# Kernel optimization log

Measured on AMD Instinct MI355X. Metric: run time of the kernel, lower is better.

## Reference

```python
import jax, jax.numpy as jnp
import numpy as np

D_MODEL = 1024
NUM_HEADS = 16
D_HEAD = D_MODEL // NUM_HEADS
SCALE = float(np.sqrt(D_HEAD))
NEG = -1e9


def setup_inputs() -> dict:
    key = jax.random.key(0)
    ks = jax.random.split(key, 4)
    B, K = 4, 1024
    tokens = jax.random.normal(ks[0], (B, K, D_MODEL), dtype=jnp.float32)
    token_mask = jnp.ones((B, K), dtype=jnp.int32)
    W_qkv = jax.random.normal(ks[1], (D_MODEL, 3 * D_MODEL), dtype=jnp.float32) * 0.02
    b_qkv = jnp.zeros((3 * D_MODEL,), dtype=jnp.float32)
    W_proj = jax.random.normal(ks[2], (D_MODEL, D_MODEL), dtype=jnp.float32) * 0.02
    b_proj = jnp.zeros((D_MODEL,), dtype=jnp.float32)
    return {"tokens": tokens, "token_mask": token_mask, "W_qkv": W_qkv,
            "b_qkv": b_qkv, "W_proj": W_proj, "b_proj": b_proj}


def reference(tokens, token_mask, W_qkv, b_qkv, W_proj, b_proj):
    B, K, D = tokens.shape
    H, dh = NUM_HEADS, D // NUM_HEADS
    # QKV projection: (B, K, 3D) -> (3, B, H, K, dh)
    qkv = (tokens @ W_qkv + b_qkv).reshape(B, K, 3, H, dh)
    qkv = jnp.transpose(qkv, (2, 0, 3, 1, 4))
    q, k, v = qkv[0], qkv[1], qkv[2]
    # scaled scores (B, H, K, K)
    attn = jnp.einsum('bhqd,bhkd->bhqk', q, k) / SCALE
    # additive padding mask: valid iff both query and key positions valid
    tm = token_mask.astype(attn.dtype)
    m = tm[:, None, None, :] * tm[:, None, :, None]          # (B,1,K,K)
    attn = attn + (1.0 - jnp.clip(m, 0.0)) * NEG
    attn = jax.nn.softmax(attn, axis=-1)
    # weighted values, merge heads
    out = jnp.einsum('bhqk,bhkd->bhqd', attn, v)
    out = jnp.transpose(out, (0, 2, 1, 3)).reshape(B, K, D)
    out = out @ W_proj + b_proj
    tokens_out = tokens + out                                 # residual (dropout=0)
    attn_out = attn.mean(axis=1)                              # (B, K, K)
    return tokens_out, attn_out
```

## Files before the change

### kernel.cpp

```cpp
#include <hip/hip_runtime.h>
#include <hip/hip_bf16.h>
#include <math.h>

#define SEQ   1024
#define DM    1024
#define NH    16
#define DH    64
#define INV_SCALE 0.125f
#define NEGBIG   -1e9f
#define MASKPEN 80.0f

typedef __attribute__((ext_vector_type(8))) __bf16 bf16x8;
typedef __attribute__((ext_vector_type(4))) float floatx4;
typedef unsigned short ushort_t;

__device__ __forceinline__ floatx4 mfma16(bf16x8 a, bf16x8 b, floatx4 c) {
    return __builtin_amdgcn_mfma_f32_16x16x32_bf16(a, b, c, 0, 0, 0);
}

__device__ __forceinline__ ushort_t f2bf(float f) {
    unsigned int u = __float_as_uint(f);
    u += 0x7fffu + ((u >> 16) & 1u);
    return (ushort_t)(u >> 16);
}

__device__ __forceinline__ void gload_lds16(const void* g, void* l) {
    __builtin_amdgcn_global_load_lds(
        (const __attribute__((address_space(1))) unsigned int*)g,
        (__attribute__((address_space(3))) unsigned int*)l, 16, 0, 0);
}

__global__ __launch_bounds__(256) void k_cast(const float* __restrict__ src,
                                              ushort_t* __restrict__ dst) {
    int i = (blockIdx.x * 256 + threadIdx.x) * 8;
    float4 a = *(const float4*)(src + i);
    float4 b = *(const float4*)(src + i + 4);
    union { ushort_t s[8]; uint4 v; } pk;
    pk.s[0] = f2bf(a.x); pk.s[1] = f2bf(a.y); pk.s[2] = f2bf(a.z); pk.s[3] = f2bf(a.w);
    pk.s[4] = f2bf(b.x); pk.s[5] = f2bf(b.y); pk.s[6] = f2bf(b.z); pk.s[7] = f2bf(b.w);
    *(uint4*)(dst + i) = pk.v;
}

__global__ __launch_bounds__(256) void k_transpose(const float* __restrict__ src,
                                                   ushort_t* __restrict__ dst,
                                                   int R, int C) {
    __shared__ ushort_t tile[32][33];
    int bx = blockIdx.x * 32;
    int by = blockIdx.y * 32;
    for (int i = threadIdx.y; i < 32; i += 8)
        tile[i][threadIdx.x] = f2bf(src[(size_t)(by + i) * C + bx + threadIdx.x]);
    __syncthreads();
    for (int i = threadIdx.y; i < 32; i += 8)
        dst[(size_t)(bx + i) * R + by + threadIdx.x] = tile[threadIdx.x][i];
}

__device__ __forceinline__ void gemm128_body(const ushort_t* __restrict__ A,
                                             const ushort_t* __restrict__ Bt,
                                             int m0, int n0, int Kd,
                                             floatx4 acc[4][4], ushort_t* smem) {
    int tid  = threadIdx.x;
    int wave = tid >> 6, lane = tid & 63;
    int l15 = lane & 15, quad = lane >> 4;
    int wr = (wave >> 1) * 64, wc = (wave & 1) * 64;
    int rsub = lane >> 2;
    int ksub = (((lane & 3) ^ ((lane >> 3) & 3)) * 8);
    int rsw  = (l15 >> 1) & 3;

    for (int k0 = 0; k0 < Kd; k0 += 32) {
        __syncthreads();
        #pragma unroll
        for (int c = 0; c < 2; ++c) {
            int rbase = wave * 32 + c * 16;
            gload_lds16(A  + (size_t)(m0 + rbase + rsub) * Kd + k0 + ksub,
                        smem + rbase * 32);
            gload_lds16(Bt + (size_t)(n0 + rbase + rsub) * Kd + k0 + ksub,
                        smem + 4096 + rbase * 32);
        }
        __syncthreads();

        bf16x8 af[4], bfr[4];
        #pragma unroll
        for (int i = 0; i < 4; ++i)
            af[i] = *(const bf16x8*)(smem + (wr + i * 16 + l15) * 32 + (quad ^ rsw) * 8);
        #pragma unroll
        for (int j = 0; j < 4; ++j)
            bfr[j] = *(const bf16x8*)(smem + 4096 + (wc + j * 16 + l15) * 32 + (quad ^ rsw) * 8);
        #pragma unroll
        for (int i = 0; i < 4; ++i)
            #pragma unroll
            for (int j = 0; j < 4; ++j)
                acc[i][j] = mfma16(af[i], bfr[j], acc[i][j]);
    }
}

__global__ __launch_bounds__(256, 2) void k_qkv_gemm(const ushort_t* __restrict__ X,
                                                     const ushort_t* __restrict__ Wt,
                                                     const float* __restrict__ bias,
                                                     ushort_t* __restrict__ qb,
                                                     ushort_t* __restrict__ kb,
                                                     ushort_t* __restrict__ vtb) {
    __shared__ ushort_t smem[8192];
    int m0 = blockIdx.y * 128, n0 = blockIdx.x * 128;
    floatx4 acc[4][4];
    #pragma unroll
    for (int i = 0; i < 4; ++i)
        #pragma unroll
        for (int j = 0; j < 4; ++j) acc[i][j] = (floatx4)0.0f;

    gemm128_body(X, Wt, m0, n0, DM, acc, smem);

    int tid = threadIdx.x, wave = tid >> 6, lane = tid & 63;
    int l15 = lane & 15, quad = lane >> 4;
    int wr = (wave >> 1) * 64, wc = (wave & 1) * 64;
    #pragma unroll
    for (int i = 0; i < 4; ++i) {
        int mrow0 = m0 + wr + i * 16 + quad * 4;
        int b = mrow0 >> 10, t0 = mrow0 & 1023;
        #pragma unroll
        for (int j = 0; j < 4; ++j) {
            int n = n0 + wc + j * 16 + l15;
            float bv = bias[n];
            int sec = n >> 10, nn = n & 1023;
            int h = nn >> 6, d = nn & 63;
            if (sec == 2) {
                union { ushort_t s[4]; uint2 v; } pk;
                #pragma unroll
                for (int r = 0; r < 4; ++r) pk.s[r] = f2bf(acc[i][j][r] + bv);
                *(uint2*)(vtb + (((size_t)(b * NH + h) * DH + d) * SEQ + t0)) = pk.v;
            } else {
                ushort_t* dst = (sec == 0) ? qb : kb;
                #pragma unroll
                for (int r = 0; r < 4; ++r)
                    dst[((size_t)(b * NH + h) * SEQ + t0 + r) * DH + d] =
                        f2bf(acc[i][j][r] + bv);
            }
        }
    }
}

__global__ __launch_bounds__(256, 4) void k_attn_flash(const ushort_t* __restrict__ qb,
                                                       const ushort_t* __restrict__ kb,
                                                       const ushort_t* __restrict__ vtb,
                                                       const int* __restrict__ mask,
                                                       float* __restrict__ lbuf,
                                                       ushort_t* __restrict__ ob) {
    __shared__ ushort_t ks[2 * 64 * 64];
    __shared__ ushort_t vs[2 * 64 * 64];
    __shared__ ushort_t ps[4 * 16 * 64];
    int bh = blockIdx.x, qt = blockIdx.y;
    int b = bh >> 4, h = bh & 15;
    int tid = threadIdx.x, wave = tid >> 6, lane = tid & 63;
    int l15 = lane & 15, quad = lane >> 4;
    int qrow = qt * 64 + wave * 16;
    ushort_t* pw = ps + wave * 1024;
    int sw7 = l15 & 7;

    int srow = wave * 16 + (lane >> 3);
    int slog = (lane & 7) ^ (srow & 7);

    const ushort_t* qbase = qb + ((size_t)bh * SEQ + qrow + l15) * DH;
    bf16x8 aq0 = *(const bf16x8*)(qbase + quad * 8);
    bf16x8 aq1 = *(const bf16x8*)(qbase + 32 + quad * 8);

    bf16x8 vones;
    #pragma unroll
    for (int i = 0; i < 8; ++i) vones[i] = (__bf16)1.0f;

    float qp[4];
    #pragma unroll
    for (int r = 0; r < 4; ++r)
        qp[r] = MASKPEN * (float)mask[b * SEQ + qrow + quad * 4 + r];

    floatx4 oacc[4], lacc = (floatx4)0.0f;
    #pragma unroll
    for (int t = 0; t < 4; ++t) oacc[t] = (floatx4)0.0f;

    #pragma unroll
    for (int c = 0; c < 2; ++c) {
        gload_lds16(kb  + ((size_t)bh * SEQ + srow + c * 8) * DH + slog * 8,
                    ks + (wave * 16 + c * 8) * 64);
        gload_lds16(vtb + ((size_t)bh * DH + srow + c * 8) * SEQ + slog * 8,
                    vs + (wave * 16 + c * 8) * 64);
    }

    for (int it = 0; it < SEQ / 64; ++it) {
        int kc = it * 64;
        int sel = it & 1;
        __syncthreads();
        if (it + 1 < SEQ / 64) {
            int nsel = sel ^ 1;
            #pragma unroll
            for (int c = 0; c < 2; ++c) {
                gload_lds16(kb  + ((size_t)bh * SEQ + kc + 64 + srow + c * 8) * DH + slog * 8,
                            ks + nsel * 4096 + (wave * 16 + c * 8) * 64);
                gload_lds16(vtb + ((size_t)bh * DH + srow + c * 8) * SEQ + kc + 64 + slog * 8,
                            vs + nsel * 4096 + (wave * 16 + c * 8) * 64);
            }
        }
        const ushort_t* kcur = ks + sel * 4096;
        const ushort_t* vcur = vs + sel * 4096;

        floatx4 s[4];
        #pragma unroll
        for (int j = 0; j < 4; ++j) {
            int row = j * 16 + l15;
            bf16x8 k0 = *(const bf16x8*)(kcur + row * 64 + ((quad ^ sw7) * 8));
            bf16x8 k1 = *(const bf16x8*)(kcur + row * 64 + (((quad + 4) ^ sw7) * 8));
            s[j] = mfma16(aq0, k0, (floatx4)0.0f);
            s[j] = mfma16(aq1, k1, s[j]);
        }
        #pragma unroll
        for (int j = 0; j < 4; ++j) {
            float km = (float)mask[b * SEQ + kc + j * 16 + l15];
            #pragma unroll
            for (int r = 0; r < 4; ++r) {
                float arg = s[j][r] * INV_SCALE + (qp[r] * km - MASKPEN);
                float p = __expf(arg);
                int rd = quad * 4 + r;
                int ch = (2 * j + (l15 >> 3)) ^ (rd & 7);
                pw[rd * 64 + ch * 8 + (l15 & 7)] = f2bf(p);
            }
        }
        bf16x8 pa0 = *(const bf16x8*)(pw + l15 * 64 + ((quad ^ sw7) * 8));
        bf16x8 pa1 = *(const bf16x8*)(pw + l15 * 64 + (((quad + 4) ^ sw7) * 8));
        lacc = mfma16(pa0, vones, lacc);
        lacc = mfma16(pa1, vones, lacc);
        #pragma unroll
        for (int t = 0; t < 4; ++t) {
            bf16x8 bv0 = *(const bf16x8*)(vcur + (t * 16 + l15) * 64 + ((quad ^ sw7) * 8));
            bf16x8 bv1 = *(const bf16x8*)(vcur + (t * 16 + l15) * 64 + (((quad + 4) ^ sw7) * 8));
            oacc[t] = mfma16(pa0, bv0, oacc[t]);
            oacc[t] = mfma16(pa1, bv1, oacc[t]);
        }
    }
    float invl[4];
    #pragma unroll
    for (int r = 0; r < 4; ++r) invl[r] = 1.0f / lacc[r];
    #pragma unroll
    for (int t = 0; t < 4; ++t)
        #pragma unroll
        for (int r = 0; r < 4; ++r)
            ob[((size_t)b * SEQ + qrow + quad * 4 + r) * DM + h * DH + t * 16 + l15] =
                f2bf(oacc[t][r] * invl[r]);
    if (l15 == 0) {
        #pragma unroll
        for (int r = 0; r < 4; ++r)
            lbuf[(size_t)bh * SEQ + qrow + quad * 4 + r] = invl[r];
    }
}

__global__ __launch_bounds__(256, 4) void k_attn_avg(const ushort_t* __restrict__ qb,
                                                     const ushort_t* __restrict__ kb,
                                                     const int* __restrict__ mask,
                                                     const float* __restrict__ lbuf,
                                                     float* __restrict__ attn_out) {
    __shared__ ushort_t ks[2 * 64 * 64];
    int bx = blockIdx.x;
    int b  = bx >> 8;
    int qt = (bx >> 4) & 15;
    int kt = bx & 15;
    int tid = threadIdx.x, wave = tid >> 6, lane = tid & 63;
    int l15 = lane & 15, quad = lane >> 4;
    int q0 = qt * 64 + wave * 16;
    int kbase = kt * 64;
    int sw7 = l15 & 7;

    int srow = wave * 16 + (lane >> 3);
    int slog = (lane & 7) ^ (srow & 7);
    int bh0 = b * NH;

    float qp[4], km[4];
    #pragma unroll
    for (int r = 0; r < 4; ++r)
        qp[r] = MASKPEN * (float)mask[b * SEQ + q0 + quad * 4 + r];
    #pragma unroll
    for (int j = 0; j < 4; ++j)
        km[j] = (float)mask[b * SEQ + kbase + j * 16 + l15];

    floatx4 aacc[4];
    #pragma unroll
    for (int j = 0; j < 4; ++j) aacc[j] = (floatx4)0.0f;

    #pragma unroll
    for (int c = 0; c < 2; ++c)
        gload_lds16(kb + ((size_t)bh0 * SEQ + kbase + srow + c * 8) * DH + slog * 8,
                    ks + (wave * 16 + c * 8) * 64);
    const ushort_t* qp0 = qb + ((size_t)bh0 * SEQ + q0 + l15) * DH;
    bf16x8 aq0 = *(const bf16x8*)(qp0 + quad * 8);
    bf16x8 aq1 = *(const bf16x8*)(qp0 + 32 + quad * 8);
    floatx4 il = *(const floatx4*)(lbuf + (size_t)bh0 * SEQ + q0 + quad * 4);
    __syncthreads();

    for (int h = 0; h < NH; ++h) {
        ushort_t* cur = ks + (h & 1) * 4096;
        ushort_t* nxt = ks + ((h + 1) & 1) * 4096;
        if (h + 1 < NH) {
            #pragma unroll
            for (int c = 0; c < 2; ++c)
                gload_lds16(kb + ((size_t)(bh0 + h + 1) * SEQ + kbase + srow + c * 8) * DH + slog * 8,
                            nxt + (wave * 16 + c * 8) * 64);
        }
        bf16x8 caq0 = aq0, caq1 = aq1;
        floatx4 cil = il;
        if (h + 1 < NH) {
            const ushort_t* qpn = qb + ((size_t)(bh0 + h + 1) * SEQ + q0 + l15) * DH;
            aq0 = *(const bf16x8*)(qpn + quad * 8);
            aq1 = *(const bf16x8*)(qpn + 32 + quad * 8);
            il = *(const floatx4*)(lbuf + (size_t)(bh0 + h + 1) * SEQ + q0 + quad * 4);
        }
        cil *= 0.0625f;

        #pragma unroll
        for (int j = 0; j < 4; ++j) {
            int row = j * 16 + l15;
            bf16x8 k0 = *(const bf16x8*)(cur + row * 64 + ((quad ^ sw7) * 8));
            bf16x8 k1 = *(const bf16x8*)(cur + row * 64 + (((quad + 4) ^ sw7) * 8));
            floatx4 s = mfma16(caq0, k0, (floatx4)0.0f);
            s = mfma16(caq1, k1, s);
            #pragma unroll
            for (int r = 0; r < 4; ++r) {
                float arg = s[r] * INV_SCALE + (qp[r] * km[j] - MASKPEN);
                aacc[j][r] += __expf(arg) * cil[r];
            }
        }
        __syncthreads();
    }
    #pragma unroll
    for (int j = 0; j < 4; ++j)
        #pragma unroll
        for (int r = 0; r < 4; ++r)
            attn_out[((size_t)b * SEQ + q0 + quad * 4 + r) * SEQ +
                     kbase + j * 16 + l15] = aacc[j][r];
}

__global__ __launch_bounds__(256, 2) void k_proj(const ushort_t* __restrict__ ob,
                                                 const ushort_t* __restrict__ Wpt,
                                                 const float* __restrict__ bias,
                                                 const float* __restrict__ tokens,
                                                 float* __restrict__ out) {
    __shared__ ushort_t smem[8192];
    int m0 = blockIdx.y * 128, n0 = blockIdx.x * 128;
    floatx4 acc[4][4];
    #pragma unroll
    for (int i = 0; i < 4; ++i)
        #pragma unroll
        for (int j = 0; j < 4; ++j) acc[i][j] = (floatx4)0.0f;

    gemm128_body(ob, Wpt, m0, n0, DM, acc, smem);

    int tid = threadIdx.x, wave = tid >> 6, lane = tid & 63;
    int l15 = lane & 15, quad = lane >> 4;
    int wr = (wave >> 1) * 64, wc = (wave & 1) * 64;
    #pragma unroll
    for (int i = 0; i < 4; ++i) {
        int m0r = m0 + wr + i * 16 + quad * 4;
        #pragma unroll
        for (int j = 0; j < 4; ++j) {
            int n = n0 + wc + j * 16 + l15;
            float bv = bias[n];
            #pragma unroll
            for (int r = 0; r < 4; ++r) {
                size_t idx = (size_t)(m0r + r) * DM + n;
                out[idx] = acc[i][j][r] + bv + tokens[idx];
            }
        }
    }
}

extern "C" void kernel_launch(void* const* d_in, const int* in_sizes, int n_in,
                              void* d_out, int out_size, void* d_ws, size_t ws_size,
                              hipStream_t stream) {
    const float* tokens = (const float*)d_in[0];
    const int*   mask   = (const int*)d_in[1];
    const float* Wqkv   = (const float*)d_in[2];
    const float* bqkv   = (const float*)d_in[3];
    const float* Wproj  = (const float*)d_in[4];
    const float* bproj  = (const float*)d_in[5];

    float* out_tok  = (float*)d_out;
    float* out_attn = out_tok + (size_t)4 * SEQ * SEQ;

    ushort_t* Xbf  = (ushort_t*)out_attn;
    ushort_t* obuf = (ushort_t*)(out_attn + (size_t)2 * SEQ * SEQ);

    ushort_t* Wt   = (ushort_t*)d_ws;
    ushort_t* Wpt  = Wt  + (size_t)3 * DM * DM;
    ushort_t* qbuf = Wpt + (size_t)DM * DM;
    ushort_t* kbuf = qbuf + (size_t)4 * SEQ * DM;
    ushort_t* vtb  = kbuf + (size_t)4 * SEQ * DM;
    float*    lbuf = (float*)(vtb + (size_t)4 * SEQ * DM);

    k_cast<<<(4 * SEQ * DM) / (8 * 256), 256, 0, stream>>>(tokens, Xbf);
    k_transpose<<<dim3(3 * DM / 32, DM / 32), dim3(32, 8), 0, stream>>>(Wqkv, Wt, DM, 3 * DM);
    k_transpose<<<dim3(DM / 32, DM / 32), dim3(32, 8), 0, stream>>>(Wproj, Wpt, DM, DM);
    k_qkv_gemm<<<dim3(24, 32), 256, 0, stream>>>(Xbf, Wt, bqkv, qbuf, kbuf, vtb);
    k_attn_flash<<<dim3(64, 16), 256, 0, stream>>>(qbuf, kbuf, vtb, mask, lbuf, obuf);
    k_proj<<<dim3(8, 32), 256, 0, stream>>>(obuf, Wpt, bproj, tokens, out_tok);
    k_attn_avg<<<1024, 256, 0, stream>>>(qbuf, kbuf, mask, lbuf, out_attn);
}
```

Before: 218.2 us.

## Merge prep kernels and co-schedule projection with attention-average kernel

```diff
diff --git a/kernel.cpp b/kernel.cpp
--- a/kernel.cpp
+++ b/kernel.cpp
@@ -30,28 +30,40 @@
         (__attribute__((address_space(3))) unsigned int*)l, 16, 0, 0);
 }
 
-__global__ __launch_bounds__(256) void k_cast(const float* __restrict__ src,
-                                              ushort_t* __restrict__ dst) {
-    int i = (blockIdx.x * 256 + threadIdx.x) * 8;
-    float4 a = *(const float4*)(src + i);
-    float4 b = *(const float4*)(src + i + 4);
-    union { ushort_t s[8]; uint4 v; } pk;
-    pk.s[0] = f2bf(a.x); pk.s[1] = f2bf(a.y); pk.s[2] = f2bf(a.z); pk.s[3] = f2bf(a.w);
-    pk.s[4] = f2bf(b.x); pk.s[5] = f2bf(b.y); pk.s[6] = f2bf(b.z); pk.s[7] = f2bf(b.w);
-    *(uint4*)(dst + i) = pk.v;
-}
-
-__global__ __launch_bounds__(256) void k_transpose(const float* __restrict__ src,
-                                                   ushort_t* __restrict__ dst,
-                                                   int R, int C) {
+__global__ __launch_bounds__(256) void k_prep(const float* __restrict__ tokens,
+                                              ushort_t* __restrict__ Xbf,
+                                              const float* __restrict__ Wqkv,
+                                              ushort_t* __restrict__ Wt,
+                                              const float* __restrict__ Wproj,
+                                              ushort_t* __restrict__ Wpt) {
     __shared__ ushort_t tile[32][33];
-    int bx = blockIdx.x * 32;
-    int by = blockIdx.y * 32;
-    for (int i = threadIdx.y; i < 32; i += 8)
-        tile[i][threadIdx.x] = f2bf(src[(size_t)(by + i) * C + bx + threadIdx.x]);
+    int bxg = blockIdx.x;
+    if (bxg < 2048) {
+        int i = (bxg * 256 + threadIdx.x) * 8;
+        float4 a = *(const float4*)(tokens + i);
+        float4 b = *(const float4*)(tokens + i + 4);
+        union { ushort_t s[8]; uint4 v; } pk;
+        pk.s[0] = f2bf(a.x); pk.s[1] = f2bf(a.y); pk.s[2] = f2bf(a.z); pk.s[3] = f2bf(a.w);
+        pk.s[4] = f2bf(b.x); pk.s[5] = f2bf(b.y); pk.s[6] = f2bf(b.z); pk.s[7] = f2bf(b.w);
+        *(uint4*)(Xbf + i) = pk.v;
+        return;
+    }
+    const float* src; ushort_t* dst; int R, C, bx, by;
+    if (bxg < 5120) {
+        int idx = bxg - 2048;
+        src = Wqkv; dst = Wt; R = DM; C = 3 * DM;
+        bx = (idx % 96) * 32; by = (idx / 96) * 32;
+    } else {
+        int idx = bxg - 5120;
+        src = Wproj; dst = Wpt; R = DM; C = DM;
+        bx = (idx % 32) * 32; by = (idx / 32) * 32;
+    }
+    int tx = threadIdx.x & 31, ty = threadIdx.x >> 5;
+    for (int i = ty; i < 32; i += 8)
+        tile[i][tx] = f2bf(src[(size_t)(by + i) * C + bx + tx]);
     __syncthreads();
-    for (int i = threadIdx.y; i < 32; i += 8)
-        dst[(size_t)(bx + i) * R + by + threadIdx.x] = tile[threadIdx.x][i];
+    for (int i = ty; i < 32; i += 8)
+        dst[(size_t)(bx + i) * R + by + tx] = tile[tx][i];
 }
 
 __device__ __forceinline__ void gemm128_body(const ushort_t* __restrict__ A,
@@ -249,13 +261,45 @@
     }
 }
 
-__global__ __launch_bounds__(256, 4) void k_attn_avg(const ushort_t* __restrict__ qb,
-                                                     const ushort_t* __restrict__ kb,
-                                                     const int* __restrict__ mask,
-                                                     const float* __restrict__ lbuf,
-                                                     float* __restrict__ attn_out) {
-    __shared__ ushort_t ks[2 * 64 * 64];
-    int bx = blockIdx.x;
+__device__ __forceinline__ void proj_body(const ushort_t* __restrict__ ob,
+                                          const ushort_t* __restrict__ Wpt,
+                                          const float* __restrict__ bias,
+                                          const float* __restrict__ tokens,
+                                          float* __restrict__ out,
+                                          int m0, int n0, ushort_t* smem) {
+    floatx4 acc[4][4];
+    #pragma unroll
+    for (int i = 0; i < 4; ++i)
+        #pragma unroll
+        for (int j = 0; j < 4; ++j) acc[i][j] = (floatx4)0.0f;
+
+    gemm128_body(ob, Wpt, m0, n0, DM, acc, smem);
+
+    int tid = threadIdx.x, wave = tid >> 6, lane = tid & 63;
+    int l15 = lane & 15, quad = lane >> 4;
+    int wr = (wave >> 1) * 64, wc = (wave & 1) * 64;
+    #pragma unroll
+    for (int i = 0; i < 4; ++i) {
+        int m0r = m0 + wr + i * 16 + quad * 4;
+        #pragma unroll
+        for (int j = 0; j < 4; ++j) {
+            int n = n0 + wc + j * 16 + l15;
+            float bv = bias[n];
+            #pragma unroll
+            for (int r = 0; r < 4; ++r) {
+                size_t idx = (size_t)(m0r + r) * DM + n;
+                out[idx] = acc[i][j][r] + bv + tokens[idx];
+            }
+        }
+    }
+}
+
+__device__ __forceinline__ void avg_body(const ushort_t* __restrict__ qb,
+                                         const ushort_t* __restrict__ kb,
+                                         const int* __restrict__ mask,
+                                         const float* __restrict__ lbuf,
+                                         float* __restrict__ attn_out,
+                                         int bx, ushort_t* ks) {
     int b  = bx >> 8;
     int qt = (bx >> 4) & 15;
     int kt = bx & 15;
@@ -333,38 +377,41 @@
                      kbase + j * 16 + l15] = aacc[j][r];
 }
 
+__global__ __launch_bounds__(256, 2) void k_proj_avg(const ushort_t* __restrict__ ob,
+                                                     const ushort_t* __restrict__ Wpt,
+                                                     const float* __restrict__ bias,
+                                                     const float* __restrict__ tokens,
+                                                     float* __restrict__ out,
+                                                     const ushort_t* __restrict__ qb,
+                                                     const ushort_t* __restrict__ kb,
+                                                     const int* __restrict__ mask,
+                                                     const float* __restrict__ lbuf,
+                                                     float* __restrict__ attn_out) {
+    __shared__ ushort_t smem[8192];
+    int bxg = blockIdx.x;
+    if (bxg < 256) {
+        proj_body(ob, Wpt, bias, tokens, out, (bxg >> 3) * 128, (bxg & 7) * 128, smem);
+    } else {
+        avg_body(qb, kb, mask, lbuf, attn_out, bxg - 256, smem);
+    }
+}
+
 __global__ __launch_bounds__(256, 2) void k_proj(const ushort_t* __restrict__ ob,
                                                  const ushort_t* __restrict__ Wpt,
                                                  const float* __restrict__ bias,
                                                  const float* __restrict__ tokens,
                                                  float* __restrict__ out) {
     __shared__ ushort_t smem[8192];
-    int m0 = blockIdx.y * 128, n0 = blockIdx.x * 128;
-    floatx4 acc[4][4];
-    #pragma unroll
-    for (int i = 0; i < 4; ++i)
-        #pragma unroll
-        for (int j = 0; j < 4; ++j) acc[i][j] = (floatx4)0.0f;
-
-    gemm128_body(ob, Wpt, m0, n0, DM, acc, smem);
-
-    int tid = threadIdx.x, wave = tid >> 6, lane = tid & 63;
-    int l15 = lane & 15, quad = lane >> 4;
-    int wr = (wave >> 1) * 64, wc = (wave & 1) * 64;
-    #pragma unroll
-    for (int i = 0; i < 4; ++i) {
-        int m0r = m0 + wr + i * 16 + quad * 4;
-        #pragma unroll
-        for (int j = 0; j < 4; ++j) {
-            int n = n0 + wc + j * 16 + l15;
-            float bv = bias[n];
-            #pragma unroll
-            for (int r = 0; r < 4; ++r) {
-                size_t idx = (size_t)(m0r + r) * DM + n;
-                out[idx] = acc[i][j][r] + bv + tokens[idx];
-            }
-        }
-    }
+    proj_body(ob, Wpt, bias, tokens, out, blockIdx.y * 128, blockIdx.x * 128, smem);
+}
+
+__global__ __launch_bounds__(256, 4) void k_attn_avg(const ushort_t* __restrict__ qb,
+                                                     const ushort_t* __restrict__ kb,
+                                                     const int* __restrict__ mask,
+                                                     const float* __restrict__ lbuf,
+                                                     float* __restrict__ attn_out) {
+    __shared__ ushort_t ks[2 * 64 * 64];
+    avg_body(qb, kb, mask, lbuf, attn_out, blockIdx.x, ks);
 }
 
 extern "C" void kernel_launch(void* const* d_in, const int* in_sizes, int n_in,
@@ -380,21 +427,28 @@
     float* out_tok  = (float*)d_out;
     float* out_attn = out_tok + (size_t)4 * SEQ * SEQ;
 
-    ushort_t* Xbf  = (ushort_t*)out_attn;
-    ushort_t* obuf = (ushort_t*)(out_attn + (size_t)2 * SEQ * SEQ);
-
     ushort_t* Wt   = (ushort_t*)d_ws;
     ushort_t* Wpt  = Wt  + (size_t)3 * DM * DM;
     ushort_t* qbuf = Wpt + (size_t)DM * DM;
     ushort_t* kbuf = qbuf + (size_t)4 * SEQ * DM;
     ushort_t* vtb  = kbuf + (size_t)4 * SEQ * DM;
     float*    lbuf = (float*)(vtb + (size_t)4 * SEQ * DM);
-
-    k_cast<<<(4 * SEQ * DM) / (8 * 256), 256, 0, stream>>>(tokens, Xbf);
-    k_transpose<<<dim3(3 * DM / 32, DM / 32), dim3(32, 8), 0, stream>>>(Wqkv, Wt, DM, 3 * DM);
-    k_transpose<<<dim3(DM / 32, DM / 32), dim3(32, 8), 0, stream>>>(Wproj, Wpt, DM, DM);
+    ushort_t* obuf_ws = (ushort_t*)(lbuf + (size_t)4 * NH * SEQ);
+    const size_t WS_NEED = 42205184;
+
+    bool big_ws = ws_size >= WS_NEED;
+    ushort_t* Xbf  = (ushort_t*)out_attn;
+    ushort_t* obuf = big_ws ? obuf_ws
+                            : (ushort_t*)(out_attn + (size_t)2 * SEQ * SEQ);
+
+    k_prep<<<6144, 256, 0, stream>>>(tokens, Xbf, Wqkv, Wt, Wproj, Wpt);
     k_qkv_gemm<<<dim3(24, 32), 256, 0, stream>>>(Xbf, Wt, bqkv, qbuf, kbuf, vtb);
     k_attn_flash<<<dim3(64, 16), 256, 0, stream>>>(qbuf, kbuf, vtb, mask, lbuf, obuf);
-    k_proj<<<dim3(8, 32), 256, 0, stream>>>(obuf, Wpt, bproj, tokens, out_tok);
-    k_attn_avg<<<1024, 256, 0, stream>>>(qbuf, kbuf, mask, lbuf, out_attn);
-}
+    if (big_ws) {
+        k_proj_avg<<<256 + 1024, 256, 0, stream>>>(obuf, Wpt, bproj, tokens, out_tok,
+                                                   qbuf, kbuf, mask, lbuf, out_attn);
+    } else {
+        k_proj<<<dim3(8, 32), 256, 0, stream>>>(obuf, Wpt, bproj, tokens, out_tok);
+        k_attn_avg<<<1024, 256, 0, stream>>>(qbuf, kbuf, mask, lbuf, out_attn);
+    }
+}
```

Result: faster. 198.9 us (-8.8%).
